# Optimization experiments

Measured on AMD Instinct MI355X. Metric: run time of the kernel, lower is better.

Reference implementation:

```python
import jax, jax.numpy as jnp
import numpy as np

HALFKP = 64 * 5 * 64          # 20480
PAD = HALFKP                  # padding row index
L1, L2, L3 = 256, 31, 32
NB = 8                        # layer-stack / psqt buckets
EMB_DIM = L1 + NB             # 264


def setup_inputs() -> dict:
    key = jax.random.key(0)
    ks = jax.random.split(key, 16)
    B = 16384
    w_idx = jax.random.randint(ks[0], (B, 32), 0, HALFKP + 1)
    b_idx = jax.random.randint(ks[1], (B, 32), 0, HALFKP + 1)
    us = jax.random.uniform(ks[2], (B,), dtype=jnp.float32)
    them = jax.random.uniform(ks[3], (B,), dtype=jnp.float32)
    piece_count = jax.random.randint(ks[4], (B,), 2, 33)
    sigma = 0.025
    emb = jax.random.uniform(ks[5], (HALFKP + 1, EMB_DIM), jnp.float32, -sigma, sigma)
    emb = emb.at[PAD].set(0.0)
    def lin(k, out_f, in_f):
        bound = 1.0 / np.sqrt(in_f)
        k1, k2 = jax.random.split(k)
        W = jax.random.uniform(k1, (out_f, in_f), jnp.float32, -bound, bound)
        b = jax.random.uniform(k2, (out_f,), jnp.float32, -bound, bound)
        return W, b
    # StackedLinear init: replicate slot-0 weights across all buckets
    w1_0, b1_0 = lin(ks[6], L2 + 1, L1)
    w1 = jnp.tile(w1_0, (NB, 1)); b1 = jnp.tile(b1_0, NB)
    fw1 = jnp.zeros((L2 + 1, L1), jnp.float32)
    fb1 = jnp.zeros((L2 + 1,), jnp.float32)
    w2_0, b2_0 = lin(ks[7], L3, L2 * 2)
    w2 = jnp.tile(w2_0, (NB, 1)); b2 = jnp.tile(b2_0, NB)
    wo_0, _ = lin(ks[8], 1, L3)
    wo = jnp.tile(wo_0, (NB, 1)); bo = jnp.zeros((NB,), jnp.float32)
    return {"emb": emb, "w1": w1, "b1": b1, "fw1": fw1, "fb1": fb1,
            "w2": w2, "b2": b2, "wo": wo, "bo": bo,
            "us": us, "them": them,
            "w_idx": w_idx, "b_idx": b_idx, "piece_count": piece_count}


def reference(emb, w1, b1, fw1, fb1, w2, b2, wo, bo, us, them,
              w_idx, b_idx, piece_count):
    emb_eff = emb.at[PAD].set(0.0)                      # padding row contributes 0
    wp = emb_eff[w_idx].sum(axis=1)                     # [B, 264]
    bp = emb_eff[b_idx].sum(axis=1)
    w, wpsqt = wp[:, :L1], wp[:, L1:]
    b, bpsqt = bp[:, :L1], bp[:, L1:]
    us_c = us[:, None]; them_c = them[:, None]
    l0 = us_c * jnp.concatenate([w, b], 1) + them_c * jnp.concatenate([b, w], 1)
    l0 = jnp.clip(l0, 0.0, 1.0)                         # [B, 512]
    h = L1 // 2
    l0 = jnp.concatenate([l0[:, :h] * l0[:, h:2*h],
                          l0[:, 2*h:3*h] * l0[:, 3*h:]], 1) * (127.0 / 128.0)  # [B,256]
    bucket = jnp.clip((piece_count - 1) // 4, 0, 7)     # [B]
    # l1: factorized stacked linear, gather the bucket's slice only
    W1 = (w1 + jnp.tile(fw1, (NB, 1))).reshape(NB, L2 + 1, L1)
    B1 = (b1 + jnp.tile(fb1, NB)).reshape(NB, L2 + 1)
    l1c = jnp.einsum('bi,bji->bj', l0, W1[bucket]) + B1[bucket]   # [B,32]
    l1x, l1x_out = l1c[:, :L2], l1c[:, L2:]
    l1x = jnp.clip(jnp.concatenate([l1x * l1x * (255.0 / 256.0), l1x], 1), 0.0, 1.0)  # [B,62]
    W2 = w2.reshape(NB, L3, L2 * 2)
    l2x = jnp.clip(jnp.einsum('bi,bji->bj', l1x, W2[bucket]) + b2.reshape(NB, L3)[bucket], 0.0, 1.0)
    Wo = wo.reshape(NB, 1, L3)
    l3c = jnp.einsum('bi,bji->bj', l2x, Wo[bucket]) + bo.reshape(NB, 1)[bucket]       # [B,1]
    fc_out = l3c + l1x_out
    bk = bucket[:, None]
    psqt_out = (jnp.take_along_axis(wpsqt, bk, 1) - jnp.take_along_axis(bpsqt, bk, 1)) * (us_c - 0.5)
    return fc_out + psqt_out                            # [B,1]
```

## Files before the change

kernel.cpp:

```cpp
#include <hip/hip_runtime.h>

#define EMBD 264
#define NROWS 20481
#define QS 5080.0f
#define INVQS (1.0f/5080.0f)

__device__ __forceinline__ float clamp01(float x) { return fminf(fmaxf(x, 0.f), 1.f); }

__global__ void prep_emb8(const float* __restrict__ emb, unsigned int* __restrict__ emb8,
                          float* __restrict__ psqt) {
    const int r = blockIdx.x;
    const int t = threadIdx.x;
    const bool pad = (r == NROWS - 1);
    const float4 v = *((const float4*)(emb + (size_t)r * EMBD) + t);
    int q0 = pad ? 128 : (int)rintf(v.x * QS) + 128;
    int q1 = pad ? 128 : (int)rintf(v.y * QS) + 128;
    int q2 = pad ? 128 : (int)rintf(v.z * QS) + 128;
    int q3 = pad ? 128 : (int)rintf(v.w * QS) + 128;
    q0 = min(max(q0, 0), 255); q1 = min(max(q1, 0), 255);
    q2 = min(max(q2, 0), 255); q3 = min(max(q3, 0), 255);
    emb8[(size_t)r * 64 + t] = (unsigned)q0 | ((unsigned)q1 << 8) |
                               ((unsigned)q2 << 16) | ((unsigned)q3 << 24);
    if (t < 8) {
        float pv = emb[(size_t)r * EMBD + 256 + t];
        psqt[r * 8 + t] = pad ? 0.f : pv;
    }
}

__global__ void prep_w1(const float* __restrict__ w1, const float* __restrict__ fw1,
                        const float* __restrict__ b1, const float* __restrict__ fb1,
                        float* __restrict__ w1c, float* __restrict__ b1c) {
    int i = blockIdx.x * 256 + threadIdx.x;
    w1c[i] = w1[i] + fw1[i & 8191];
    if (i < 256) b1c[i] = b1[i] + fb1[i & 31];
}

__global__ __launch_bounds__(256) void nnue_fwd_i8(
    const unsigned int* __restrict__ emb8,
    const float* __restrict__ psqt,
    const float* __restrict__ w1c,
    const float* __restrict__ b1c,
    const float* __restrict__ w2,
    const float* __restrict__ b2,
    const float* __restrict__ wo,
    const float* __restrict__ bo,
    const float* __restrict__ us,
    const float* __restrict__ them,
    const int*   __restrict__ w_idx,
    const int*   __restrict__ b_idx,
    const int*   __restrict__ pcnt,
    float* __restrict__ out,
    int B)
{
    const int lane = threadIdx.x & 63;
    const int row  = blockIdx.x * 4 + (threadIdx.x >> 6);
    if (row >= B) return;

    const float usv = us[row];
    const float thv = them[row];
    int bucket = (pcnt[row] - 1) >> 2;
    bucket = bucket > 7 ? 7 : bucket;
    bucket = __builtin_amdgcn_readfirstlane(bucket);

    const int kk = lane & 31;
    const int myidx = (lane < 32) ? w_idx[row * 32 + kk] : b_idx[row * 32 + kk];

    float ps = psqt[myidx * 8 + bucket];
    ps += __shfl_xor(ps, 16);
    ps += __shfl_xor(ps, 8);
    ps += __shfl_xor(ps, 4);
    ps += __shfl_xor(ps, 2);
    ps += __shfl_xor(ps, 1);
    const float psq_w = __shfl(ps, 0);
    const float psq_b = __shfl(ps, 32);

    unsigned aw0 = 0, aw1 = 0, ab0 = 0, ab1 = 0;
    const unsigned M = 0x00FF00FFu;
#pragma unroll
    for (int kb = 0; kb < 32; kb += 8) {
        unsigned vw[8], vb[8];
#pragma unroll
        for (int k = 0; k < 8; ++k) {
            const int iw = __shfl(myidx, kb + k);
            const int ib = __shfl(myidx, 32 + kb + k);
            vw[k] = emb8[(size_t)iw * 64 + lane];
            vb[k] = emb8[(size_t)ib * 64 + lane];
        }
#pragma unroll
        for (int k = 0; k < 8; ++k) {
            aw0 += vw[k] & M; aw1 += (vw[k] >> 8) & M;
            ab0 += vb[k] & M; ab1 += (vb[k] >> 8) & M;
        }
    }
    float4 aw, ab;
    aw.x = ((int)(aw0 & 0xffffu) - 4096) * INVQS;
    aw.y = ((int)(aw1 & 0xffffu) - 4096) * INVQS;
    aw.z = ((int)(aw0 >> 16)     - 4096) * INVQS;
    aw.w = ((int)(aw1 >> 16)     - 4096) * INVQS;
    ab.x = ((int)(ab0 & 0xffffu) - 4096) * INVQS;
    ab.y = ((int)(ab1 & 0xffffu) - 4096) * INVQS;
    ab.z = ((int)(ab0 >> 16)     - 4096) * INVQS;
    ab.w = ((int)(ab1 >> 16)     - 4096) * INVQS;

    float4 p, q;
    p.x = clamp01(usv * aw.x + thv * ab.x);
    p.y = clamp01(usv * aw.y + thv * ab.y);
    p.z = clamp01(usv * aw.z + thv * ab.z);
    p.w = clamp01(usv * aw.w + thv * ab.w);
    q.x = clamp01(usv * ab.x + thv * aw.x);
    q.y = clamp01(usv * ab.y + thv * aw.y);
    q.z = clamp01(usv * ab.z + thv * aw.z);
    q.w = clamp01(usv * ab.w + thv * aw.w);

    float4 po, qo;
    po.x = __shfl_xor(p.x, 32); po.y = __shfl_xor(p.y, 32);
    po.z = __shfl_xor(p.z, 32); po.w = __shfl_xor(p.w, 32);
    qo.x = __shfl_xor(q.x, 32); qo.y = __shfl_xor(q.y, 32);
    qo.z = __shfl_xor(q.z, 32); qo.w = __shfl_xor(q.w, 32);
    const float c127 = 127.f / 128.f;
    float4 l0f;
    if (lane < 32) {
        l0f.x = p.x * po.x * c127; l0f.y = p.y * po.y * c127;
        l0f.z = p.z * po.z * c127; l0f.w = p.w * po.w * c127;
    } else {
        l0f.x = q.x * qo.x * c127; l0f.y = q.y * qo.y * c127;
        l0f.z = q.z * qo.z * c127; l0f.w = q.w * qo.w * c127;
    }

    float part[32];
    const float4* w1p = (const float4*)(w1c + (size_t)bucket * 8192);
#pragma unroll
    for (int j = 0; j < 32; ++j) {
        const float4 wv = w1p[j * 64 + lane];
        part[j] = l0f.x * wv.x + l0f.y * wv.y + l0f.z * wv.z + l0f.w * wv.w;
    }
#pragma unroll
    for (int j = 0; j < 32; ++j) {
        float v = part[j];
        v += __shfl_xor(v, 32);
        v += __shfl_xor(v, 16);
        v += __shfl_xor(v, 8);
        v += __shfl_xor(v, 4);
        v += __shfl_xor(v, 2);
        v += __shfl_xor(v, 1);
        part[j] = v + b1c[bucket * 32 + j];
    }

    const float l1x_out = part[31];

    float acc2 = 0.f;
    if (lane < 32) {
        const float* w2r = w2 + (size_t)(bucket * 32 + lane) * 62;
#pragma unroll
        for (int i = 0; i < 31; ++i) {
            const float a  = part[i];
            const float sq = clamp01(a * a * (255.f / 256.f));
            const float ln = clamp01(a);
            acc2 += sq * w2r[i];
            acc2 += ln * w2r[31 + i];
        }
        acc2 += b2[bucket * 32 + lane];
        acc2 = clamp01(acc2) * wo[bucket * 32 + lane];
    }
    acc2 += __shfl_xor(acc2, 16);
    acc2 += __shfl_xor(acc2, 8);
    acc2 += __shfl_xor(acc2, 4);
    acc2 += __shfl_xor(acc2, 2);
    acc2 += __shfl_xor(acc2, 1);

    if (lane == 0) {
        out[row] = acc2 + bo[bucket] + l1x_out + (psq_w - psq_b) * (usv - 0.5f);
    }
}

__global__ __launch_bounds__(256) void nnue_fwd_f32(
    const float* __restrict__ emb,
    const float* __restrict__ w1e, const float* __restrict__ fw1,
    const float* __restrict__ b1e, const float* __restrict__ fb1,
    const float* __restrict__ w2,  const float* __restrict__ b2,
    const float* __restrict__ wo,  const float* __restrict__ bo,
    const float* __restrict__ us,  const float* __restrict__ them,
    const int* __restrict__ w_idx, const int* __restrict__ b_idx,
    const int* __restrict__ pcnt,  float* __restrict__ out, int B)
{
    const int lane = threadIdx.x & 63;
    const int row  = blockIdx.x * 4 + (threadIdx.x >> 6);
    if (row >= B) return;
    const float usv = us[row];
    const float thv = them[row];
    int bucket = (pcnt[row] - 1) >> 2;
    bucket = bucket > 7 ? 7 : bucket;
    bucket = __builtin_amdgcn_readfirstlane(bucket);
    const int kk = lane & 31;
    const int myidx = (lane < 32) ? w_idx[row * 32 + kk] : b_idx[row * 32 + kk];
    float ps = emb[(size_t)myidx * EMBD + 256 + bucket];
    ps += __shfl_xor(ps, 16); ps += __shfl_xor(ps, 8);
    ps += __shfl_xor(ps, 4);  ps += __shfl_xor(ps, 2); ps += __shfl_xor(ps, 1);
    const float psq_w = __shfl(ps, 0);
    const float psq_b = __shfl(ps, 32);
    float4 aw = make_float4(0,0,0,0), ab = make_float4(0,0,0,0);
#pragma unroll
    for (int k = 0; k < 32; ++k) {
        const int iw = __shfl(myidx, k);
        const int ib = __shfl(myidx, 32 + k);
        const float4 vw = *((const float4*)(emb + (size_t)iw * EMBD) + lane);
        const float4 vb = *((const float4*)(emb + (size_t)ib * EMBD) + lane);
        aw.x += vw.x; aw.y += vw.y; aw.z += vw.z; aw.w += vw.w;
        ab.x += vb.x; ab.y += vb.y; ab.z += vb.z; ab.w += vb.w;
    }
    float4 p, q;
    p.x = clamp01(usv*aw.x + thv*ab.x); p.y = clamp01(usv*aw.y + thv*ab.y);
    p.z = clamp01(usv*aw.z + thv*ab.z); p.w = clamp01(usv*aw.w + thv*ab.w);
    q.x = clamp01(usv*ab.x + thv*aw.x); q.y = clamp01(usv*ab.y + thv*aw.y);
    q.z = clamp01(usv*ab.z + thv*aw.z); q.w = clamp01(usv*ab.w + thv*aw.w);
    float4 po, qo;
    po.x = __shfl_xor(p.x,32); po.y = __shfl_xor(p.y,32);
    po.z = __shfl_xor(p.z,32); po.w = __shfl_xor(p.w,32);
    qo.x = __shfl_xor(q.x,32); qo.y = __shfl_xor(q.y,32);
    qo.z = __shfl_xor(q.z,32); qo.w = __shfl_xor(q.w,32);
    const float c127 = 127.f/128.f;
    float4 l0f;
    if (lane < 32) { l0f.x=p.x*po.x*c127; l0f.y=p.y*po.y*c127; l0f.z=p.z*po.z*c127; l0f.w=p.w*po.w*c127; }
    else           { l0f.x=q.x*qo.x*c127; l0f.y=q.y*qo.y*c127; l0f.z=q.z*qo.z*c127; l0f.w=q.w*qo.w*c127; }
    float part[32];
    const float4* w1p = (const float4*)(w1e + (size_t)bucket * 8192);
    const float4* f1p = fw1 ? (const float4*)fw1 : nullptr;
#pragma unroll
    for (int j = 0; j < 32; ++j) {
        float4 wv = w1p[j*64 + lane];
        if (f1p) { float4 fv = f1p[j*64 + lane]; wv.x+=fv.x; wv.y+=fv.y; wv.z+=fv.z; wv.w+=fv.w; }
        part[j] = l0f.x*wv.x + l0f.y*wv.y + l0f.z*wv.z + l0f.w*wv.w;
    }
#pragma unroll
    for (int j = 0; j < 32; ++j) {
        float v = part[j];
        v += __shfl_xor(v,32); v += __shfl_xor(v,16); v += __shfl_xor(v,8);
        v += __shfl_xor(v,4);  v += __shfl_xor(v,2);  v += __shfl_xor(v,1);
        v += b1e[bucket*32 + j];
        if (fb1) v += fb1[j];
        part[j] = v;
    }
    const float l1x_out = part[31];
    float acc2 = 0.f;
    if (lane < 32) {
        const float* w2r = w2 + (size_t)(bucket*32 + lane) * 62;
#pragma unroll
        for (int i = 0; i < 31; ++i) {
            const float a = part[i];
            acc2 += clamp01(a*a*(255.f/256.f)) * w2r[i];
            acc2 += clamp01(a) * w2r[31+i];
        }
        acc2 += b2[bucket*32 + lane];
        acc2 = clamp01(acc2) * wo[bucket*32 + lane];
    }
    acc2 += __shfl_xor(acc2,16); acc2 += __shfl_xor(acc2,8);
    acc2 += __shfl_xor(acc2,4);  acc2 += __shfl_xor(acc2,2); acc2 += __shfl_xor(acc2,1);
    if (lane == 0)
        out[row] = acc2 + bo[bucket] + l1x_out + (psq_w - psq_b) * (usv - 0.5f);
}

extern "C" void kernel_launch(void* const* d_in, const int* in_sizes, int n_in,
                              void* d_out, int out_size, void* d_ws, size_t ws_size,
                              hipStream_t stream) {
    const float* emb  = (const float*)d_in[0];
    const float* w1   = (const float*)d_in[1];
    const float* b1   = (const float*)d_in[2];
    const float* fw1  = (const float*)d_in[3];
    const float* fb1  = (const float*)d_in[4];
    const float* w2   = (const float*)d_in[5];
    const float* b2   = (const float*)d_in[6];
    const float* wo   = (const float*)d_in[7];
    const float* bo   = (const float*)d_in[8];
    const float* us   = (const float*)d_in[9];
    const float* them = (const float*)d_in[10];
    const int*   wi   = (const int*)d_in[11];
    const int*   bi   = (const int*)d_in[12];
    const int*   pc   = (const int*)d_in[13];
    float* out = (float*)d_out;

    const int B = in_sizes[9];
    const int grid = (B + 3) / 4;

    const size_t emb8_bytes = (size_t)NROWS * 64 * 4;
    const size_t psqt_bytes = (size_t)NROWS * 8 * 4;
    const size_t need_i8    = emb8_bytes + psqt_bytes + (65536 + 256) * 4;
    const size_t need_f32   = (size_t)(65536 + 256) * 4;

    if (ws_size >= need_i8) {
        unsigned int* emb8 = (unsigned int*)d_ws;
        float* psqt = (float*)((char*)d_ws + emb8_bytes);
        float* w1c  = (float*)((char*)d_ws + emb8_bytes + psqt_bytes);
        float* b1c  = w1c + 65536;
        prep_emb8<<<NROWS, 64, 0, stream>>>(emb, emb8, psqt);
        prep_w1<<<256, 256, 0, stream>>>(w1, fw1, b1, fb1, w1c, b1c);
        nnue_fwd_i8<<<grid, 256, 0, stream>>>(emb8, psqt, w1c, b1c,
                                              w2, b2, wo, bo, us, them, wi, bi, pc, out, B);
    } else if (ws_size >= need_f32) {
        float* w1c = (float*)d_ws;
        float* b1c = w1c + 65536;
        prep_w1<<<256, 256, 0, stream>>>(w1, fw1, b1, fb1, w1c, b1c);
        nnue_fwd_f32<<<grid, 256, 0, stream>>>(emb, w1c, nullptr, b1c, nullptr,
                                               w2, b2, wo, bo, us, them, wi, bi, pc, out, B);
    } else {
        nnue_fwd_f32<<<grid, 256, 0, stream>>>(emb, w1, fw1, b1, fb1,
                                               w2, b2, wo, bo, us, them, wi, bi, pc, out, B);
    }
}
```

Measured before the change: 157.7 us.

## Compute L1 layer with bf16 MFMA over 16-row tiles across all buckets

Each block now gathers and quantizes embeddings for 16 rows, stores the bf16 L0 activations in LDS, and computes the L1 layer with bf16 MFMA 16x16x32 against every one of the 8 buckets. Each row then picks its own bucket's result from LDS for the L2 and output layers. This replaces per-row shuffle-reduction dot products, trading 8x redundant L1 compute and bf16 rounding for matrix-core throughput. It also prepacks the W1 table into MFMA layout and pads W2, and prep_emb8 now processes four rows per block.

```diff
diff --git a/kernel.cpp b/kernel.cpp
--- a/kernel.cpp
+++ b/kernel.cpp
@@ -5,12 +5,21 @@
 #define QS 5080.0f
 #define INVQS (1.0f/5080.0f)
 
+typedef short short8 __attribute__((ext_vector_type(8)));
+typedef float f32x4  __attribute__((ext_vector_type(4)));
+
 __device__ __forceinline__ float clamp01(float x) { return fminf(fmaxf(x, 0.f), 1.f); }
+__device__ __forceinline__ unsigned short f2bf(float f) {
+    unsigned u = __float_as_uint(f);
+    u += 0x7fffu + ((u >> 16) & 1u);
+    return (unsigned short)(u >> 16);
+}
 
 __global__ void prep_emb8(const float* __restrict__ emb, unsigned int* __restrict__ emb8,
                           float* __restrict__ psqt) {
-    const int r = blockIdx.x;
-    const int t = threadIdx.x;
+    const int r = blockIdx.x * 4 + (threadIdx.x >> 6);
+    const int t = threadIdx.x & 63;
+    if (r >= NROWS) return;
     const bool pad = (r == NROWS - 1);
     const float4 v = *((const float4*)(emb + (size_t)r * EMBD) + t);
     int q0 = pad ? 128 : (int)rintf(v.x * QS) + 128;
@@ -27,20 +36,37 @@
     }
 }
 
-__global__ void prep_w1(const float* __restrict__ w1, const float* __restrict__ fw1,
-                        const float* __restrict__ b1, const float* __restrict__ fb1,
-                        float* __restrict__ w1c, float* __restrict__ b1c) {
-    int i = blockIdx.x * 256 + threadIdx.x;
-    w1c[i] = w1[i] + fw1[i & 8191];
-    if (i < 256) b1c[i] = b1[i] + fb1[i & 31];
-}
-
-__global__ __launch_bounds__(256) void nnue_fwd_i8(
+__global__ void prep_tables(const float* __restrict__ w1, const float* __restrict__ fw1,
+                            const float* __restrict__ b1, const float* __restrict__ fb1,
+                            const float* __restrict__ w2,
+                            unsigned short* __restrict__ w1b, float* __restrict__ b1c,
+                            float* __restrict__ w2p) {
+    const int e = blockIdx.x * 256 + threadIdx.x;
+    const int bkt = e >> 13, rem = e & 8191;
+    const int s = rem >> 10, rem2 = rem & 1023;
+    const int nt = rem2 >> 9, rem3 = rem2 & 511;
+    const int ln = rem3 >> 3, j = rem3 & 7;
+    const int n  = nt * 16 + (ln & 15);
+    const int hi = ln >> 4;
+    const int k  = s * 32 + hi * 8 + j;
+    const float v = w1[(bkt * 32 + n) * 256 + k] + fw1[n * 256 + k];
+    w1b[e] = f2bf(v);
+    if (e < 256) b1c[e] = b1[e] + fb1[e & 31];
+    if (e < 16384) {
+        const int jr = e >> 6, i = e & 63;
+        float x = 0.f;
+        if (i < 31) x = w2[jr * 62 + i];
+        else if (i >= 32 && i < 63) x = w2[jr * 62 + i - 1];
+        w2p[e] = x;
+    }
+}
+
+__global__ __launch_bounds__(256) void nnue_fwd_mfma(
     const unsigned int* __restrict__ emb8,
     const float* __restrict__ psqt,
-    const float* __restrict__ w1c,
+    const unsigned short* __restrict__ w1b,
     const float* __restrict__ b1c,
-    const float* __restrict__ w2,
+    const float* __restrict__ w2p,
     const float* __restrict__ b2,
     const float* __restrict__ wo,
     const float* __restrict__ bo,
@@ -52,124 +78,182 @@
     float* __restrict__ out,
     int B)
 {
-    const int lane = threadIdx.x & 63;
-    const int row  = blockIdx.x * 4 + (threadIdx.x >> 6);
-    if (row >= B) return;
-
-    const float usv = us[row];
-    const float thv = them[row];
-    int bucket = (pcnt[row] - 1) >> 2;
-    bucket = bucket > 7 ? 7 : bucket;
-    bucket = __builtin_amdgcn_readfirstlane(bucket);
-
-    const int kk = lane & 31;
-    const int myidx = (lane < 32) ? w_idx[row * 32 + kk] : b_idx[row * 32 + kk];
-
-    float ps = psqt[myidx * 8 + bucket];
-    ps += __shfl_xor(ps, 16);
-    ps += __shfl_xor(ps, 8);
-    ps += __shfl_xor(ps, 4);
-    ps += __shfl_xor(ps, 2);
-    ps += __shfl_xor(ps, 1);
-    const float psq_w = __shfl(ps, 0);
-    const float psq_b = __shfl(ps, 32);
-
-    unsigned aw0 = 0, aw1 = 0, ab0 = 0, ab1 = 0;
-    const unsigned M = 0x00FF00FFu;
-#pragma unroll
-    for (int kb = 0; kb < 32; kb += 8) {
-        unsigned vw[8], vb[8];
-#pragma unroll
-        for (int k = 0; k < 8; ++k) {
-            const int iw = __shfl(myidx, kb + k);
-            const int ib = __shfl(myidx, 32 + kb + k);
-            vw[k] = emb8[(size_t)iw * 64 + lane];
-            vb[k] = emb8[(size_t)ib * 64 + lane];
-        }
-#pragma unroll
-        for (int k = 0; k < 8; ++k) {
-            aw0 += vw[k] & M; aw1 += (vw[k] >> 8) & M;
-            ab0 += vb[k] & M; ab1 += (vb[k] >> 8) & M;
-        }
-    }
-    float4 aw, ab;
-    aw.x = ((int)(aw0 & 0xffffu) - 4096) * INVQS;
-    aw.y = ((int)(aw1 & 0xffffu) - 4096) * INVQS;
-    aw.z = ((int)(aw0 >> 16)     - 4096) * INVQS;
-    aw.w = ((int)(aw1 >> 16)     - 4096) * INVQS;
-    ab.x = ((int)(ab0 & 0xffffu) - 4096) * INVQS;
-    ab.y = ((int)(ab1 & 0xffffu) - 4096) * INVQS;
-    ab.z = ((int)(ab0 >> 16)     - 4096) * INVQS;
-    ab.w = ((int)(ab1 >> 16)     - 4096) * INVQS;
-
-    float4 p, q;
-    p.x = clamp01(usv * aw.x + thv * ab.x);
-    p.y = clamp01(usv * aw.y + thv * ab.y);
-    p.z = clamp01(usv * aw.z + thv * ab.z);
-    p.w = clamp01(usv * aw.w + thv * ab.w);
-    q.x = clamp01(usv * ab.x + thv * aw.x);
-    q.y = clamp01(usv * ab.y + thv * aw.y);
-    q.z = clamp01(usv * ab.z + thv * aw.z);
-    q.w = clamp01(usv * ab.w + thv * aw.w);
-
-    float4 po, qo;
-    po.x = __shfl_xor(p.x, 32); po.y = __shfl_xor(p.y, 32);
-    po.z = __shfl_xor(p.z, 32); po.w = __shfl_xor(p.w, 32);
-    qo.x = __shfl_xor(q.x, 32); qo.y = __shfl_xor(q.y, 32);
-    qo.z = __shfl_xor(q.z, 32); qo.w = __shfl_xor(q.w, 32);
-    const float c127 = 127.f / 128.f;
-    float4 l0f;
-    if (lane < 32) {
-        l0f.x = p.x * po.x * c127; l0f.y = p.y * po.y * c127;
-        l0f.z = p.z * po.z * c127; l0f.w = p.w * po.w * c127;
-    } else {
-        l0f.x = q.x * qo.x * c127; l0f.y = q.y * qo.y * c127;
-        l0f.z = q.z * qo.z * c127; l0f.w = q.w * qo.w * c127;
-    }
-
-    float part[32];
-    const float4* w1p = (const float4*)(w1c + (size_t)bucket * 8192);
-#pragma unroll
-    for (int j = 0; j < 32; ++j) {
-        const float4 wv = w1p[j * 64 + lane];
-        part[j] = l0f.x * wv.x + l0f.y * wv.y + l0f.z * wv.z + l0f.w * wv.w;
-    }
-#pragma unroll
-    for (int j = 0; j < 32; ++j) {
-        float v = part[j];
-        v += __shfl_xor(v, 32);
-        v += __shfl_xor(v, 16);
-        v += __shfl_xor(v, 8);
-        v += __shfl_xor(v, 4);
-        v += __shfl_xor(v, 2);
-        v += __shfl_xor(v, 1);
-        part[j] = v + b1c[bucket * 32 + j];
-    }
-
-    const float l1x_out = part[31];
-
-    float acc2 = 0.f;
-    if (lane < 32) {
-        const float* w2r = w2 + (size_t)(bucket * 32 + lane) * 62;
-#pragma unroll
-        for (int i = 0; i < 31; ++i) {
-            const float a  = part[i];
-            const float sq = clamp01(a * a * (255.f / 256.f));
-            const float ln = clamp01(a);
-            acc2 += sq * w2r[i];
-            acc2 += ln * w2r[31 + i];
-        }
-        acc2 += b2[bucket * 32 + lane];
-        acc2 = clamp01(acc2) * wo[bucket * 32 + lane];
-    }
-    acc2 += __shfl_xor(acc2, 16);
-    acc2 += __shfl_xor(acc2, 8);
-    acc2 += __shfl_xor(acc2, 4);
-    acc2 += __shfl_xor(acc2, 2);
-    acc2 += __shfl_xor(acc2, 1);
-
-    if (lane == 0) {
-        out[row] = acc2 + bo[bucket] + l1x_out + (psq_w - psq_b) * (usv - 0.5f);
+    __shared__ unsigned short A_lds[16 * 280];
+    __shared__ float l1c[8 * 16 * 36];
+    __shared__ float psq_lds[16];
+    __shared__ int   bkt_lds[16];
+
+    const int tid  = threadIdx.x;
+    const int lane = tid & 63;
+    const int w    = tid >> 6;
+
+    for (int rr = 0; rr < 4; ++rr) {
+        const int m = w * 4 + rr;
+        int grow = blockIdx.x * 16 + m;
+        const bool valid = grow < B;
+        if (!valid) grow = B - 1;
+
+        const float usv = us[grow];
+        const float thv = them[grow];
+        int bucket = (pcnt[grow] - 1) >> 2;
+        bucket = bucket > 7 ? 7 : bucket;
+        bucket = __builtin_amdgcn_readfirstlane(bucket);
+
+        const int kk = lane & 31;
+        const int myidx = (lane < 32) ? w_idx[grow * 32 + kk] : b_idx[grow * 32 + kk];
+
+        float ps = psqt[myidx * 8 + bucket];
+        ps += __shfl_xor(ps, 16);
+        ps += __shfl_xor(ps, 8);
+        ps += __shfl_xor(ps, 4);
+        ps += __shfl_xor(ps, 2);
+        ps += __shfl_xor(ps, 1);
+        const float psq_w = __shfl(ps, 0);
+        const float psq_b = __shfl(ps, 32);
+
+        unsigned aw0 = 0, aw1 = 0, ab0 = 0, ab1 = 0;
+        const unsigned M = 0x00FF00FFu;
+#pragma unroll
+        for (int kb = 0; kb < 32; kb += 8) {
+            unsigned vw[8], vb[8];
+#pragma unroll
+            for (int k2 = 0; k2 < 8; ++k2) {
+                const int iw = __shfl(myidx, kb + k2);
+                const int ib = __shfl(myidx, 32 + kb + k2);
+                vw[k2] = emb8[(size_t)iw * 64 + lane];
+                vb[k2] = emb8[(size_t)ib * 64 + lane];
+            }
+#pragma unroll
+            for (int k2 = 0; k2 < 8; ++k2) {
+                aw0 += vw[k2] & M; aw1 += (vw[k2] >> 8) & M;
+                ab0 += vb[k2] & M; ab1 += (vb[k2] >> 8) & M;
+            }
+        }
+        float4 aw, ab;
+        aw.x = ((int)(aw0 & 0xffffu) - 4096) * INVQS;
+        aw.y = ((int)(aw1 & 0xffffu) - 4096) * INVQS;
+        aw.z = ((int)(aw0 >> 16)     - 4096) * INVQS;
+        aw.w = ((int)(aw1 >> 16)     - 4096) * INVQS;
+        ab.x = ((int)(ab0 & 0xffffu) - 4096) * INVQS;
+        ab.y = ((int)(ab1 & 0xffffu) - 4096) * INVQS;
+        ab.z = ((int)(ab0 >> 16)     - 4096) * INVQS;
+        ab.w = ((int)(ab1 >> 16)     - 4096) * INVQS;
+
+        float4 p, q;
+        p.x = clamp01(usv * aw.x + thv * ab.x);
+        p.y = clamp01(usv * aw.y + thv * ab.y);
+        p.z = clamp01(usv * aw.z + thv * ab.z);
+        p.w = clamp01(usv * aw.w + thv * ab.w);
+        q.x = clamp01(usv * ab.x + thv * aw.x);
+        q.y = clamp01(usv * ab.y + thv * aw.y);
+        q.z = clamp01(usv * ab.z + thv * aw.z);
+        q.w = clamp01(usv * ab.w + thv * aw.w);
+
+        float4 po, qo;
+        po.x = __shfl_xor(p.x, 32); po.y = __shfl_xor(p.y, 32);
+        po.z = __shfl_xor(p.z, 32); po.w = __shfl_xor(p.w, 32);
+        qo.x = __shfl_xor(q.x, 32); qo.y = __shfl_xor(q.y, 32);
+        qo.z = __shfl_xor(q.z, 32); qo.w = __shfl_xor(q.w, 32);
+        const float c127 = 127.f / 128.f;
+        float4 l0f;
+        if (lane < 32) {
+            l0f.x = p.x * po.x * c127; l0f.y = p.y * po.y * c127;
+            l0f.z = p.z * po.z * c127; l0f.w = p.w * po.w * c127;
+        } else {
+            l0f.x = q.x * qo.x * c127; l0f.y = q.y * qo.y * c127;
+            l0f.z = q.z * qo.z * c127; l0f.w = q.w * qo.w * c127;
+        }
+
+        const unsigned lo  = (unsigned)f2bf(l0f.x) | ((unsigned)f2bf(l0f.y) << 16);
+        const unsigned hi2 = (unsigned)f2bf(l0f.z) | ((unsigned)f2bf(l0f.w) << 16);
+        *((unsigned long long*)&A_lds[m * 280 + lane * 4]) =
+            ((unsigned long long)hi2 << 32) | (unsigned long long)lo;
+        if (lane == 0) {
+            psq_lds[m] = (psq_w - psq_b) * (usv - 0.5f);
+            bkt_lds[m] = bucket;
+        }
+    }
+    __syncthreads();
+
+    {
+        const int col = lane & 15;
+        const int hi  = lane >> 4;
+        f32x4 acc[2][2];
+#pragma unroll
+        for (int bb = 0; bb < 2; ++bb)
+#pragma unroll
+            for (int nt = 0; nt < 2; ++nt)
+                acc[bb][nt] = (f32x4){0.f, 0.f, 0.f, 0.f};
+
+#pragma unroll
+        for (int s = 0; s < 8; ++s) {
+            const short8 a = *((const short8*)&A_lds[col * 280 + s * 32 + hi * 8]);
+#pragma unroll
+            for (int bb = 0; bb < 2; ++bb) {
+                const int bkt = w * 2 + bb;
+#pragma unroll
+                for (int nt = 0; nt < 2; ++nt) {
+                    const short8 bf = *((const short8*)&w1b[(((bkt * 8 + s) * 2 + nt) * 64 + lane) * 8]);
+                    acc[bb][nt] = __builtin_amdgcn_mfma_f32_16x16x32_bf16(a, bf, acc[bb][nt], 0, 0, 0);
+                }
+            }
+        }
+#pragma unroll
+        for (int bb = 0; bb < 2; ++bb) {
+            const int bkt = w * 2 + bb;
+#pragma unroll
+            for (int nt = 0; nt < 2; ++nt) {
+                const float bias = b1c[bkt * 32 + nt * 16 + col];
+#pragma unroll
+                for (int reg = 0; reg < 4; ++reg) {
+                    const int mr = hi * 4 + reg;
+                    l1c[(bkt * 16 + mr) * 36 + nt * 16 + col] = acc[bb][nt][reg] + bias;
+                }
+            }
+        }
+    }
+    __syncthreads();
+
+    {
+        const int row = tid >> 4;
+        const int jj  = tid & 15;
+        const int bkt = bkt_lds[row];
+        const float4* crow = (const float4*)&l1c[(bkt * 16 + row) * 36];
+        float4 c4[8];
+#pragma unroll
+        for (int b5 = 0; b5 < 8; ++b5) c4[b5] = crow[b5];
+
+        const float4* wr0 = (const float4*)&w2p[(bkt * 32 + jj) * 64];
+        const float4* wr1 = (const float4*)&w2p[(bkt * 32 + jj + 16) * 64];
+        float acc0 = 0.f, acc1 = 0.f;
+        const float kq = 255.f / 256.f;
+#pragma unroll
+        for (int b5 = 0; b5 < 8; ++b5) {
+            const float4 cv = c4[b5];
+            float4 sq, ln;
+            sq.x = clamp01(cv.x * cv.x * kq); ln.x = clamp01(cv.x);
+            sq.y = clamp01(cv.y * cv.y * kq); ln.y = clamp01(cv.y);
+            sq.z = clamp01(cv.z * cv.z * kq); ln.z = clamp01(cv.z);
+            sq.w = clamp01(cv.w * cv.w * kq); ln.w = clamp01(cv.w);
+            const float4 ws0 = wr0[b5], wl0 = wr0[8 + b5];
+            const float4 ws1 = wr1[b5], wl1 = wr1[8 + b5];
+            acc0 += sq.x * ws0.x + sq.y * ws0.y + sq.z * ws0.z + sq.w * ws0.w;
+            acc0 += ln.x * wl0.x + ln.y * wl0.y + ln.z * wl0.z + ln.w * wl0.w;
+            acc1 += sq.x * ws1.x + sq.y * ws1.y + sq.z * ws1.z + sq.w * ws1.w;
+            acc1 += ln.x * wl1.x + ln.y * wl1.y + ln.z * wl1.z + ln.w * wl1.w;
+        }
+        const float t0 = clamp01(acc0 + b2[bkt * 32 + jj])      * wo[bkt * 32 + jj];
+        const float t1 = clamp01(acc1 + b2[bkt * 32 + jj + 16]) * wo[bkt * 32 + jj + 16];
+        float t = t0 + t1;
+        t += __shfl_xor(t, 8);
+        t += __shfl_xor(t, 4);
+        t += __shfl_xor(t, 2);
+        t += __shfl_xor(t, 1);
+        if (jj == 0) {
+            const int grow = blockIdx.x * 16 + row;
+            if (grow < B)
+                out[grow] = t + bo[bkt] + c4[7].w + psq_lds[row];
+        }
     }
 }
 
@@ -224,11 +308,12 @@
     else           { l0f.x=q.x*qo.x*c127; l0f.y=q.y*qo.y*c127; l0f.z=q.z*qo.z*c127; l0f.w=q.w*qo.w*c127; }
     float part[32];
     const float4* w1p = (const float4*)(w1e + (size_t)bucket * 8192);
-    const float4* f1p = fw1 ? (const float4*)fw1 : nullptr;
+    const float4* f1p = (const float4*)fw1;
 #pragma unroll
     for (int j = 0; j < 32; ++j) {
         float4 wv = w1p[j*64 + lane];
-        if (f1p) { float4 fv = f1p[j*64 + lane]; wv.x+=fv.x; wv.y+=fv.y; wv.z+=fv.z; wv.w+=fv.w; }
+        float4 fv = f1p[j*64 + lane];
+        wv.x+=fv.x; wv.y+=fv.y; wv.z+=fv.z; wv.w+=fv.w;
         part[j] = l0f.x*wv.x + l0f.y*wv.y + l0f.z*wv.z + l0f.w*wv.w;
     }
 #pragma unroll
@@ -236,9 +321,7 @@
         float v = part[j];
         v += __shfl_xor(v,32); v += __shfl_xor(v,16); v += __shfl_xor(v,8);
         v += __shfl_xor(v,4);  v += __shfl_xor(v,2);  v += __shfl_xor(v,1);
-        v += b1e[bucket*32 + j];
-        if (fb1) v += fb1[j];
-        part[j] = v;
+        part[j] = v + b1e[bucket*32 + j] + fb1[j];
     }
     const float l1x_out = part[31];
     float acc2 = 0.f;
@@ -279,30 +362,28 @@
     float* out = (float*)d_out;
 
     const int B = in_sizes[9];
-    const int grid = (B + 3) / 4;
-
-    const size_t emb8_bytes = (size_t)NROWS * 64 * 4;
+
+    const size_t emb8_bytes = (size_t)NROWS * 256;
     const size_t psqt_bytes = (size_t)NROWS * 8 * 4;
-    const size_t need_i8    = emb8_bytes + psqt_bytes + (65536 + 256) * 4;
-    const size_t need_f32   = (size_t)(65536 + 256) * 4;
-
-    if (ws_size >= need_i8) {
-        unsigned int* emb8 = (unsigned int*)d_ws;
-        float* psqt = (float*)((char*)d_ws + emb8_bytes);
-        float* w1c  = (float*)((char*)d_ws + emb8_bytes + psqt_bytes);
-        float* b1c  = w1c + 65536;
-        prep_emb8<<<NROWS, 64, 0, stream>>>(emb, emb8, psqt);
-        prep_w1<<<256, 256, 0, stream>>>(w1, fw1, b1, fb1, w1c, b1c);
-        nnue_fwd_i8<<<grid, 256, 0, stream>>>(emb8, psqt, w1c, b1c,
-                                              w2, b2, wo, bo, us, them, wi, bi, pc, out, B);
-    } else if (ws_size >= need_f32) {
-        float* w1c = (float*)d_ws;
-        float* b1c = w1c + 65536;
-        prep_w1<<<256, 256, 0, stream>>>(w1, fw1, b1, fb1, w1c, b1c);
-        nnue_fwd_f32<<<grid, 256, 0, stream>>>(emb, w1c, nullptr, b1c, nullptr,
-                                               w2, b2, wo, bo, us, them, wi, bi, pc, out, B);
+    const size_t w1b_bytes  = 65536 * 2;
+    const size_t b1c_bytes  = 256 * 4;
+    const size_t w2p_bytes  = 16384 * 4;
+    const size_t need = emb8_bytes + psqt_bytes + w1b_bytes + b1c_bytes + w2p_bytes;
+
+    if (ws_size >= need && (B % 16) == 0) {
+        char* p = (char*)d_ws;
+        unsigned int*   emb8 = (unsigned int*)p;            p += emb8_bytes;
+        float*          psqt = (float*)p;                   p += psqt_bytes;
+        unsigned short* w1b  = (unsigned short*)p;          p += w1b_bytes;
+        float*          b1c  = (float*)p;                   p += b1c_bytes;
+        float*          w2p  = (float*)p;
+
+        prep_emb8<<<(NROWS + 3) / 4, 256, 0, stream>>>(emb, emb8, psqt);
+        prep_tables<<<256, 256, 0, stream>>>(w1, fw1, b1, fb1, w2, w1b, b1c, w2p);
+        nnue_fwd_mfma<<<B / 16, 256, 0, stream>>>(emb8, psqt, w1b, b1c, w2p,
+                                                  b2, wo, bo, us, them, wi, bi, pc, out, B);
     } else {
-        nnue_fwd_f32<<<grid, 256, 0, stream>>>(emb, w1, fw1, b1, fb1,
-                                               w2, b2, wo, bo, us, them, wi, bi, pc, out, B);
-    }
-}
+        nnue_fwd_f32<<<(B + 3) / 4, 256, 0, stream>>>(emb, w1, fw1, b1, fb1,
+                                                      w2, b2, wo, bo, us, them, wi, bi, pc, out, B);
+    }
+}
```

Measured after the change: 141.7 us. 1.11x faster.
